# Optimization experiments

Hardware: AMD Instinct MI355X
Metric: run time of the kernel (lower is better)

Reference implementation:

```python
import jax, jax.numpy as jnp
import numpy as np

B, T, H, DK = 4, 2048, 16, 64
F = H * DK
CK, NL = 64, 16  # chunk_size, num left chunks
MIN_VAL = float(np.finfo(np.float16).min)


def chunk_mask(size, ck, nl):
    # row i attends cols [max((i//ck - nl)*ck, 0), (i//ck + 1)*ck)
    i = jnp.arange(size)
    start = jnp.maximum((i // ck - nl) * ck, 0)
    end = (i // ck + 1) * ck
    j = jnp.arange(size)
    return (j[None, :] >= start[:, None]) & (j[None, :] < end[:, None])


def setup_inputs() -> dict:
    rng = jax.random.key(0)
    ks = jax.random.split(rng, 14)
    s = 1.0 / np.sqrt(F)
    mask = jnp.broadcast_to(chunk_mask(T, CK, NL)[None], (B, T, T))  # padding mask all-True & chunk band
    return {
        "query": jax.random.normal(ks[0], (B, T, F), jnp.float32),
        "key": jax.random.normal(ks[1], (B, T, F), jnp.float32),
        "value": jax.random.normal(ks[2], (B, T, F), jnp.float32),
        "pos_emb": jax.random.normal(ks[3], (1, T, F), jnp.float32),
        "mask": mask,
        "Wq": jax.random.normal(ks[4], (F, F), jnp.float32) * s,
        "bq": jnp.zeros((F,), jnp.float32),
        "Wk": jax.random.normal(ks[5], (F, F), jnp.float32) * s,
        "bk": jnp.zeros((F,), jnp.float32),
        "Wv": jax.random.normal(ks[6], (F, F), jnp.float32) * s,
        "bv": jnp.zeros((F,), jnp.float32),
        "Wp": jax.random.normal(ks[7], (F, F), jnp.float32) * s,
        "Wo": jax.random.normal(ks[8], (F, F), jnp.float32) * s,
        "bo": jnp.zeros((F,), jnp.float32),
        "pos_bias_u": jax.random.normal(ks[9], (H, DK), jnp.float32) * 0.05,
        "pos_bias_v": jax.random.normal(ks[10], (H, DK), jnp.float32) * 0.05,
    }


def reference(query, key, value, pos_emb, mask, Wq, bq, Wk, bk, Wv, bv, Wp, Wo, bo, pos_bias_u, pos_bias_v):
    b, t1, _ = query.shape
    t2 = key.shape[1]
    q = (query @ Wq.T + bq).reshape(b, t1, H, DK)            # (b, t1, h, d)
    k = (key @ Wk.T + bk).reshape(b, t2, H, DK).transpose(0, 2, 1, 3)   # (b, h, t2, d)
    v = (value @ Wv.T + bv).reshape(b, t2, H, DK).transpose(0, 2, 1, 3)  # (b, h, t2, d)
    p = (pos_emb @ Wp.T).reshape(pos_emb.shape[0], -1, H, DK).transpose(0, 2, 1, 3)[0]  # (h, t2, d)
    # matrix_ac: content score with bias u; matrix_bd: position score with bias v (no rel_shift in forward)
    matrix_ac = jnp.einsum('bthd,bhsd->bhts', q + pos_bias_u, k)
    matrix_bd = jnp.einsum('bthd,hsd->bhts', q + pos_bias_v, p)
    scores = (matrix_ac + matrix_bd) / np.sqrt(DK)
    m = mask[:, None, :, :]                                   # (b, 1, t1, t2)
    scores = jnp.where(m, scores, MIN_VAL)
    attn = jax.nn.softmax(scores, axis=-1)
    attn = jnp.where(m, attn, 0.0)
    x = jnp.einsum('bhts,bhsd->bthd', attn, v).reshape(b, t1, F)
    return x @ Wo.T + bo
```

## Files before the change

### kernel.cpp

```cpp
#include <hip/hip_runtime.h>
#include <hip/hip_bf16.h>

#define B_ 4
#define T_ 2048
#define H_ 16
#define DK_ 64
#define F_ 1024
#define SCALE_LOG2 0.18033688011112042f

typedef __bf16 bf16x8 __attribute__((ext_vector_type(8)));
typedef __bf16 bf16x4 __attribute__((ext_vector_type(4)));
typedef float f32x4 __attribute__((ext_vector_type(4)));

__device__ __forceinline__ void async_cp16(const void* g, void* l) {
  __builtin_amdgcn_global_load_lds((const __attribute__((address_space(1))) void*)g,
                                   (__attribute__((address_space(3))) void*)l, 16, 0, 0);
}

struct CvtArgs {
  const float* src[9];
  __bf16* dst[9];
  int n[9];
};
__global__ void cvt_all(CvtArgs a) {
  int t = blockIdx.y;
  int i = (blockIdx.x * 256 + threadIdx.x) * 8;
  if (i >= a.n[t]) return;
  const float* in = a.src[t];
  __bf16* out = a.dst[t];
  float4 x = *(const float4*)(in + i);
  float4 y = *(const float4*)(in + i + 4);
  bf16x8 o;
  o[0] = (__bf16)x.x; o[1] = (__bf16)x.y; o[2] = (__bf16)x.z; o[3] = (__bf16)x.w;
  o[4] = (__bf16)y.x; o[5] = (__bf16)y.y; o[6] = (__bf16)y.z; o[7] = (__bf16)y.w;
  *(bf16x8*)(out + i) = o;
}

struct G8 {
  const __bf16* A[4];
  const __bf16* Bm[4];
  const float* bias[4];
  __bf16* out[4];
  int nx[4];
};

__global__ __launch_bounds__(512, 2) void gemm_qkvp8(G8 g) {
  const int z = blockIdx.z;
  if ((int)blockIdx.x >= g.nx[z]) return;
  constexpr int K = F_;
  constexpr int NT = K / 64;
  __shared__ __bf16 LDS[65536];
  const __bf16* __restrict__ A = g.A[z];
  const __bf16* __restrict__ Bmm = g.Bm[z];
  const float* __restrict__ bias = g.bias[z];
  __bf16* __restrict__ Co = g.out[z];
  const int tid = threadIdx.x;
  const int wave = tid >> 6, lane = tid & 63;
  const int mrow = lane & 15, quad = lane >> 4;
  const int wm = wave >> 2, wn = wave & 3;
  const long m0 = (long)blockIdx.y * 256;
  const long n0 = (long)blockIdx.x * 256;
  const int srow = tid >> 3;
  const int sslot = tid & 7;
  const int scol = ((sslot ^ (srow & 7)) * 8);
  const __bf16* sA = A + (m0 + srow) * K + scol;
  const __bf16* sB = Bmm + (n0 + srow) * K + scol;
  const int ldsw = wave * 512;
  const int csw0 = ((quad) ^ (mrow & 7)) * 8;
  const int csw1 = ((4 + quad) ^ (mrow & 7)) * 8;

#define STAGE_A(t_, h_)                                              \
  do {                                                               \
    __bf16* lb_ = &LDS[(((t_)&1) * 2 + (h_)) * 8192 + ldsw];         \
    const __bf16* ga_ = sA + (h_) * (128 * K) + (t_)*64;             \
    async_cp16(ga_, lb_);                                            \
    async_cp16(ga_ + 64 * K, lb_ + 4096);                            \
  } while (0)
#define STAGE_B(t_, h_)                                              \
  do {                                                               \
    __bf16* lb_ = &LDS[32768 + (((t_)&1) * 2 + (h_)) * 8192 + ldsw]; \
    const __bf16* gb_ = sB + (h_) * (128 * K) + (t_)*64;             \
    async_cp16(gb_, lb_);                                            \
    async_cp16(gb_ + 64 * K, lb_ + 4096);                            \
  } while (0)

  f32x4 acc[8][4] = {};
  bf16x8 af[8][2], bf[4][2];
  STAGE_A(0, 0); STAGE_A(0, 1); STAGE_B(0, 0); STAGE_B(0, 1);
  STAGE_A(1, 0); STAGE_A(1, 1);

#pragma unroll 2
  for (int t = 0; t < NT; ++t) {
    const int d = t & 1;
    const __bf16* Ab = &LDS[(d * 2 + wm) * 8192];
    const __bf16* Bb = &LDS[32768 + (d * 2 + (wn >> 1)) * 8192 + (wn & 1) * 4096];
    if (t + 1 < NT) {
      STAGE_B(t + 1, 0);
      asm volatile("s_waitcnt vmcnt(6)" ::: "memory");
    } else {
      asm volatile("s_waitcnt vmcnt(0)" ::: "memory");
    }
    __builtin_amdgcn_s_barrier();
#pragma unroll
    for (int fr = 0; fr < 4; ++fr) {
      af[fr][0] = *(const bf16x8*)&Ab[(fr * 16 + mrow) * 64 + csw0];
      af[fr][1] = *(const bf16x8*)&Ab[(fr * 16 + mrow) * 64 + csw1];
    }
#pragma unroll
    for (int fc = 0; fc < 2; ++fc) {
      bf[fc][0] = *(const bf16x8*)&Bb[(fc * 16 + mrow) * 64 + csw0];
      bf[fc][1] = *(const bf16x8*)&Bb[(fc * 16 + mrow) * 64 + csw1];
    }
    __builtin_amdgcn_s_setprio(1);
#pragma unroll
    for (int fr = 0; fr < 4; ++fr)
#pragma unroll
      for (int fc = 0; fc < 2; ++fc) {
        acc[fr][fc] = __builtin_amdgcn_mfma_f32_16x16x32_bf16(af[fr][0], bf[fc][0], acc[fr][fc], 0, 0, 0);
        acc[fr][fc] = __builtin_amdgcn_mfma_f32_16x16x32_bf16(af[fr][1], bf[fc][1], acc[fr][fc], 0, 0, 0);
      }
    __builtin_amdgcn_s_setprio(0);
    __builtin_amdgcn_s_barrier();
    if (t + 1 < NT) STAGE_B(t + 1, 1);
#pragma unroll
    for (int fr = 4; fr < 8; ++fr) {
      af[fr][0] = *(const bf16x8*)&Ab[(fr * 16 + mrow) * 64 + csw0];
      af[fr][1] = *(const bf16x8*)&Ab[(fr * 16 + mrow) * 64 + csw1];
    }
#pragma unroll
    for (int fc = 2; fc < 4; ++fc) {
      bf[fc][0] = *(const bf16x8*)&Bb[(fc * 16 + mrow) * 64 + csw0];
      bf[fc][1] = *(const bf16x8*)&Bb[(fc * 16 + mrow) * 64 + csw1];
    }
    __builtin_amdgcn_s_setprio(1);
#pragma unroll
    for (int fr = 4; fr < 8; ++fr)
#pragma unroll
      for (int fc = 2; fc < 4; ++fc) {
        acc[fr][fc] = __builtin_amdgcn_mfma_f32_16x16x32_bf16(af[fr][0], bf[fc][0], acc[fr][fc], 0, 0, 0);
        acc[fr][fc] = __builtin_amdgcn_mfma_f32_16x16x32_bf16(af[fr][1], bf[fc][1], acc[fr][fc], 0, 0, 0);
      }
    __builtin_amdgcn_s_setprio(0);
    __builtin_amdgcn_s_barrier();
    if (t + 2 < NT) STAGE_A(t + 2, 0);
    __builtin_amdgcn_s_setprio(1);
#pragma unroll
    for (int fr = 0; fr < 4; ++fr)
#pragma unroll
      for (int fc = 2; fc < 4; ++fc) {
        acc[fr][fc] = __builtin_amdgcn_mfma_f32_16x16x32_bf16(af[fr][0], bf[fc][0], acc[fr][fc], 0, 0, 0);
        acc[fr][fc] = __builtin_amdgcn_mfma_f32_16x16x32_bf16(af[fr][1], bf[fc][1], acc[fr][fc], 0, 0, 0);
      }
    __builtin_amdgcn_s_setprio(0);
    __builtin_amdgcn_s_barrier();
    if (t + 2 < NT) STAGE_A(t + 2, 1);
    __builtin_amdgcn_s_setprio(1);
#pragma unroll
    for (int fr = 4; fr < 8; ++fr)
#pragma unroll
      for (int fc = 0; fc < 2; ++fc) {
        acc[fr][fc] = __builtin_amdgcn_mfma_f32_16x16x32_bf16(af[fr][0], bf[fc][0], acc[fr][fc], 0, 0, 0);
        acc[fr][fc] = __builtin_amdgcn_mfma_f32_16x16x32_bf16(af[fr][1], bf[fc][1], acc[fr][fc], 0, 0, 0);
      }
    __builtin_amdgcn_s_setprio(0);
    __builtin_amdgcn_s_barrier();
  }
#undef STAGE_A
#undef STAGE_B

#pragma unroll
  for (int fr = 0; fr < 8; ++fr) {
    int frow = (int)m0 + wm * 128 + fr * 16 + quad * 4;
    float4 b4 = bias ? *(const float4*)&bias[frow] : make_float4(0.f, 0.f, 0.f, 0.f);
    int h = frow >> 6, dbase = frow & 63;
#pragma unroll
    for (int fc = 0; fc < 4; ++fc) {
      int token = (int)n0 + wn * 64 + fc * 16 + mrow;
      int bb = token >> 11, tt = token & 2047;
      bf16x4 pk;
      pk[0] = (__bf16)(acc[fr][fc][0] + b4.x);
      pk[1] = (__bf16)(acc[fr][fc][1] + b4.y);
      pk[2] = (__bf16)(acc[fr][fc][2] + b4.z);
      pk[3] = (__bf16)(acc[fr][fc][3] + b4.w);
      *(bf16x4*)&Co[(((long)(bb * H_ + h)) * T_ + tt) * DK_ + dbase] = pk;
    }
  }
}

__global__ __launch_bounds__(256) void gemm_out(
    const __bf16* __restrict__ A, const __bf16* __restrict__ Bm,
    float* __restrict__ Cout, const float* __restrict__ bias, int N, int K) {
  __shared__ __bf16 As[128 * 32];
  __shared__ __bf16 Bs[128 * 32];
  const int tid = threadIdx.x;
  const int wave = tid >> 6, lane = tid & 63;
  const int mrow = lane & 15, quad = lane >> 4;
  const long m0 = (long)blockIdx.y * 128, n0 = (long)blockIdx.x * 128;
  const int wr = (wave >> 1) * 64, wc = (wave & 1) * 64;
  const int srow = lane >> 2;
  const int scol = (lane & 3) * 8;
  f32x4 acc[4][4] = {};
  for (int k0 = 0; k0 < K; k0 += 32) {
    if (k0) __syncthreads();
    for (int ph = 0; ph < 2; ++ph) {
      int rb = ph * 64 + wave * 16;
      async_cp16(A + (m0 + rb + srow) * (long)K + k0 + scol, As + rb * 32);
      async_cp16(Bm + (n0 + rb + srow) * (long)K + k0 + scol, Bs + rb * 32);
    }
    __syncthreads();
    bf16x8 af[4], bf[4];
    for (int i = 0; i < 4; i++) af[i] = *(const bf16x8*)&As[(wr + i * 16 + mrow) * 32 + quad * 8];
    for (int j = 0; j < 4; j++) bf[j] = *(const bf16x8*)&Bs[(wc + j * 16 + mrow) * 32 + quad * 8];
    for (int i = 0; i < 4; i++)
      for (int j = 0; j < 4; j++)
        acc[i][j] = __builtin_amdgcn_mfma_f32_16x16x32_bf16(af[i], bf[j], acc[i][j], 0, 0, 0);
  }
  for (int i = 0; i < 4; i++) {
    int row = (int)m0 + wr + i * 16 + quad * 4;
    for (int j = 0; j < 4; j++) {
      int col = (int)n0 + wc + j * 16 + mrow;
      float bval = bias[col];
      for (int r = 0; r < 4; r++)
        Cout[(long)(row + r) * N + col] = acc[i][j][r] + bval;
    }
  }
}

__global__ __launch_bounds__(256) void prep(
    const __bf16* __restrict__ Ph, __bf16* __restrict__ Kh,
    const __bf16* __restrict__ Vh, __bf16* __restrict__ Vth,
    const float* __restrict__ u, const float* __restrict__ vb,
    float* __restrict__ biasC) {
  __shared__ __bf16 Vl[64 * 72];
  const int tc = blockIdx.x, h = blockIdx.y, b = blockIdx.z;
  const int tid = threadIdx.x;
  const int r4 = tid >> 2, c16 = (tid & 3) * 16;
  const long bh = b * H_ + h;
  const long kbase = (bh * T_ + tc * 64 + r4) * DK_ + c16;
  const long pbase = (((long)h) * T_ + tc * 64 + r4) * DK_ + c16;
  bf16x8 k0 = *(const bf16x8*)&Kh[kbase];
  bf16x8 k1 = *(const bf16x8*)&Kh[kbase + 8];
  bf16x8 p0 = *(const bf16x8*)&Ph[pbase];
  bf16x8 p1 = *(const bf16x8*)&Ph[pbase + 8];
  float4 u0 = *(const float4*)&u[h * 64 + c16];
  float4 u1 = *(const float4*)&u[h * 64 + c16 + 4];
  float4 u2 = *(const float4*)&u[h * 64 + c16 + 8];
  float4 u3 = *(const float4*)&u[h * 64 + c16 + 12];
  float4 v0 = *(const float4*)&vb[h * 64 + c16];
  float4 v1 = *(const float4*)&vb[h * 64 + c16 + 4];
  float4 v2 = *(const float4*)&vb[h * 64 + c16 + 8];
  float4 v3 = *(const float4*)&vb[h * 64 + c16 + 12];
  float s = 0.f;
  {
    const float uu[16] = {u0.x,u0.y,u0.z,u0.w,u1.x,u1.y,u1.z,u1.w,u2.x,u2.y,u2.z,u2.w,u3.x,u3.y,u3.z,u3.w};
    const float vv[16] = {v0.x,v0.y,v0.z,v0.w,v1.x,v1.y,v1.z,v1.w,v2.x,v2.y,v2.z,v2.w,v3.x,v3.y,v3.z,v3.w};
#pragma unroll
    for (int j = 0; j < 8; j++) {
      s += (float)k0[j] * uu[j] + (float)p0[j] * vv[j];
      s += (float)k1[j] * uu[8 + j] + (float)p1[j] * vv[8 + j];
    }
  }
  bf16x8 kp0, kp1;
#pragma unroll
  for (int j = 0; j < 8; j++) {
    kp0[j] = (__bf16)((float)k0[j] + (float)p0[j]);
    kp1[j] = (__bf16)((float)k1[j] + (float)p1[j]);
  }
  *(bf16x8*)&Kh[kbase] = kp0;
  *(bf16x8*)&Kh[kbase + 8] = kp1;
  s += __shfl_xor(s, 1);
  s += __shfl_xor(s, 2);
  if ((tid & 3) == 0) biasC[bh * T_ + tc * 64 + r4] = s * SCALE_LOG2;
  const long vbase = (bh * T_ + tc * 64 + r4) * DK_ + c16;
  bf16x8 vv0 = *(const bf16x8*)&Vh[vbase];
  bf16x8 vv1 = *(const bf16x8*)&Vh[vbase + 8];
  *(bf16x8*)&Vl[r4 * 72 + c16] = vv0;
  *(bf16x8*)&Vl[r4 * 72 + c16 + 8] = vv1;
  __syncthreads();
  const int d4 = tid >> 2, tcol = (tid & 3) * 16;
  bf16x8 o0, o1;
#pragma unroll
  for (int j = 0; j < 8; j++) {
    o0[j] = Vl[(tcol + j) * 72 + d4];
    o1[j] = Vl[(tcol + 8 + j) * 72 + d4];
  }
  long obase = (bh * DK_ + d4) * T_ + tc * 64 + tcol;
  *(bf16x8*)&Vth[obase] = o0;
  *(bf16x8*)&Vth[obase + 8] = o1;
}

template <int FULL>
__device__ __forceinline__ void attn_step2(
    int s0, long bh, int tid, int wave, int mrow, int quad,
    const __bf16* __restrict__ Kh, const __bf16* __restrict__ Vth,
    const float* __restrict__ Bp, const bf16x8 (&qf)[4][2],
    __bf16* Pl, __bf16* Vt, f32x4 accO[4], f32x4& accL) {
  __syncthreads();
  if (FULL) {
#pragma unroll
    for (int p = 0; p < 4; ++p) {
      int idx = tid + p * 256;
      int row = idx >> 4, colg = (idx & 15) * 8;
      *(bf16x8*)&Vt[row * 136 + colg] =
          *(const bf16x8*)&Vth[(bh * DK_ + row) * T_ + s0 + colg];
    }
  } else {
#pragma unroll
    for (int p = 0; p < 2; ++p) {
      int idx = tid + p * 256;
      int row = idx >> 3, colg = (idx & 7) * 8;
      *(bf16x8*)&Vt[row * 136 + colg] =
          *(const bf16x8*)&Vth[(bh * DK_ + row) * T_ + s0 + colg];
    }
  }
  if (FULL || wave < 2) {
    const int krow = s0 + wave * 32;
    bf16x8 kf[2][2];
#pragma unroll
    for (int nt = 0; nt < 2; ++nt)
#pragma unroll
      for (int kh = 0; kh < 2; ++kh)
        kf[nt][kh] = *(const bf16x8*)&Kh[(bh * T_ + krow + nt * 16 + mrow) * DK_ + kh * 32 + quad * 8];
    float bias01[2] = {Bp[krow + mrow], Bp[krow + 16 + mrow]};
    f32x4 s[4][2];
#pragma unroll
    for (int mt = 0; mt < 4; ++mt)
#pragma unroll
      for (int nt = 0; nt < 2; ++nt) {
        f32x4 a = {0.f, 0.f, 0.f, 0.f};
        a = __builtin_amdgcn_mfma_f32_16x16x32_bf16(qf[mt][0], kf[nt][0], a, 0, 0, 0);
        a = __builtin_amdgcn_mfma_f32_16x16x32_bf16(qf[mt][1], kf[nt][1], a, 0, 0, 0);
        s[mt][nt] = a;
      }
#pragma unroll
    for (int mt = 0; mt < 4; ++mt)
#pragma unroll
      for (int nt = 0; nt < 2; ++nt)
#pragma unroll
        for (int r = 0; r < 4; ++r) {
          float p = __builtin_amdgcn_exp2f(s[mt][nt][r] * SCALE_LOG2 + bias01[nt]);
          Pl[(mt * 16 + quad * 4 + r) * 136 + wave * 32 + nt * 16 + mrow] = (__bf16)p;
        }
  }
  __syncthreads();
  constexpr int NKT = FULL ? 4 : 2;
  bf16x8 ones;
#pragma unroll
  for (int j = 0; j < 8; ++j) ones[j] = (__bf16)1.0f;
  bf16x8 ap[NKT];
#pragma unroll
  for (int kt = 0; kt < NKT; ++kt)
    ap[kt] = *(const bf16x8*)&Pl[(wave * 16 + mrow) * 136 + kt * 32 + quad * 8];
#pragma unroll
  for (int kt = 0; kt < NKT; ++kt) {
    accL = __builtin_amdgcn_mfma_f32_16x16x32_bf16(ap[kt], ones, accL, 0, 0, 0);
#pragma unroll
    for (int nt = 0; nt < 4; ++nt) {
      bf16x8 bv = *(const bf16x8*)&Vt[(nt * 16 + mrow) * 136 + kt * 32 + quad * 8];
      accO[nt] = __builtin_amdgcn_mfma_f32_16x16x32_bf16(ap[kt], bv, accO[nt], 0, 0, 0);
    }
  }
}

__global__ __launch_bounds__(256) void attn_banded(
    const __bf16* __restrict__ Qh, const __bf16* __restrict__ Kh,
    const __bf16* __restrict__ Vth, const float* __restrict__ biasC,
    __bf16* __restrict__ X) {
  __shared__ __bf16 Pl[64 * 136];
  __shared__ __bf16 Vt[64 * 136];
  const int qc = blockIdx.x, h = blockIdx.y, b = blockIdx.z;
  const int tid = threadIdx.x, wave = tid >> 6, lane = tid & 63;
  const int mrow = lane & 15, quad = lane >> 4;
  const long bh = b * H_ + h;
  const int span = (qc >= 16 ? 17 : qc + 1);
  const int s_lo = (qc + 1 - span) * 64, s_hi = (qc + 1) * 64;
  const float* Bp = biasC + bh * T_;
  bf16x8 qf[4][2];
#pragma unroll
  for (int mt = 0; mt < 4; ++mt)
#pragma unroll
    for (int kh = 0; kh < 2; ++kh)
      qf[mt][kh] = *(const bf16x8*)&Qh[(bh * T_ + qc * 64 + mt * 16 + mrow) * DK_ + kh * 32 + quad * 8];
  f32x4 accO[4] = {};
  f32x4 accL = {0.f, 0.f, 0.f, 0.f};
  int s0 = s_lo;
  if (span & 1) {
    attn_step2<0>(s0, bh, tid, wave, mrow, quad, Kh, Vth, Bp, qf, Pl, Vt, accO, accL);
    s0 += 64;
  }
  for (; s0 < s_hi; s0 += 128)
    attn_step2<1>(s0, bh, tid, wave, mrow, quad, Kh, Vth, Bp, qf, Pl, Vt, accO, accL);
#pragma unroll
  for (int r = 0; r < 4; ++r) {
    float inv = 1.0f / accL[r];
    int t = qc * 64 + wave * 16 + quad * 4 + r;
#pragma unroll
    for (int nt = 0; nt < 4; ++nt)
      X[((long)(b * T_ + t) * H_ + h) * DK_ + nt * 16 + mrow] = (__bf16)(accO[nt][r] * inv);
  }
}

extern "C" void kernel_launch(void* const* d_in, const int* in_sizes, int n_in,
                              void* d_out, int out_size, void* d_ws, size_t ws_size,
                              hipStream_t stream) {
  (void)in_sizes; (void)n_in; (void)out_size; (void)ws_size;
  const float* query = (const float*)d_in[0];
  const float* key   = (const float*)d_in[1];
  const float* value = (const float*)d_in[2];
  const float* pos   = (const float*)d_in[3];
  const float* Wq = (const float*)d_in[5];
  const float* bq = (const float*)d_in[6];
  const float* Wk = (const float*)d_in[7];
  const float* bk = (const float*)d_in[8];
  const float* Wv = (const float*)d_in[9];
  const float* bv = (const float*)d_in[10];
  const float* Wp = (const float*)d_in[11];
  const float* Wo = (const float*)d_in[12];
  const float* bo = (const float*)d_in[13];
  const float* pu = (const float*)d_in[14];
  const float* pvb = (const float*)d_in[15];

  const long NQ = (long)B_ * T_ * F_;
  const long NP = (long)T_ * F_;
  const long NW = (long)F_ * F_;
  char* ws = (char*)d_ws;
  __bf16* qb  = (__bf16*)ws; ws += NQ * 2;
  __bf16* kb  = (__bf16*)ws; ws += NQ * 2;
  __bf16* vbm = (__bf16*)ws; ws += NQ * 2;
  __bf16* pb  = (__bf16*)ws; ws += NP * 2;
  __bf16* wqb = (__bf16*)ws; ws += NW * 2;
  __bf16* wkb = (__bf16*)ws; ws += NW * 2;
  __bf16* wvb = (__bf16*)ws; ws += NW * 2;
  __bf16* wpb = (__bf16*)ws; ws += NW * 2;
  __bf16* wob = (__bf16*)ws; ws += NW * 2;
  __bf16* Qh  = (__bf16*)ws; ws += NQ * 2;
  __bf16* Kh  = (__bf16*)ws; ws += NQ * 2;
  __bf16* Vh  = (__bf16*)ws; ws += NQ * 2;
  __bf16* Ph  = (__bf16*)ws; ws += NP * 2;
  float*  biasC = (float*)ws; ws += (long)B_ * H_ * T_ * 4;
  __bf16* Vth = kb;
  __bf16* Xb  = qb;

  {
    CvtArgs ca;
    ca.src[0] = query; ca.dst[0] = qb;  ca.n[0] = (int)NQ;
    ca.src[1] = key;   ca.dst[1] = kb;  ca.n[1] = (int)NQ;
    ca.src[2] = value; ca.dst[2] = vbm; ca.n[2] = (int)NQ;
    ca.src[3] = pos;   ca.dst[3] = pb;  ca.n[3] = (int)NP;
    ca.src[4] = Wq;    ca.dst[4] = wqb; ca.n[4] = (int)NW;
    ca.src[5] = Wk;    ca.dst[5] = wkb; ca.n[5] = (int)NW;
    ca.src[6] = Wv;    ca.dst[6] = wvb; ca.n[6] = (int)NW;
    ca.src[7] = Wp;    ca.dst[7] = wpb; ca.n[7] = (int)NW;
    ca.src[8] = Wo;    ca.dst[8] = wob; ca.n[8] = (int)NW;
    cvt_all<<<dim3(4096, 9), 256, 0, stream>>>(ca);
  }
  {
    G8 g;
    g.A[0] = wqb; g.Bm[0] = qb;  g.bias[0] = bq;      g.out[0] = Qh; g.nx[0] = 32;
    g.A[1] = wkb; g.Bm[1] = kb;  g.bias[1] = bk;      g.out[1] = Kh; g.nx[1] = 32;
    g.A[2] = wvb; g.Bm[2] = vbm; g.bias[2] = bv;      g.out[2] = Vh; g.nx[2] = 32;
    g.A[3] = wpb; g.Bm[3] = pb;  g.bias[3] = nullptr; g.out[3] = Ph; g.nx[3] = 8;
    gemm_qkvp8<<<dim3(32, 4, 4), 512, 0, stream>>>(g);
  }
  prep<<<dim3(32, 16, 4), 256, 0, stream>>>(Ph, Kh, Vh, Vth, pu, pvb, biasC);
  attn_banded<<<dim3(32, 16, 4), 256, 0, stream>>>(Qh, Kh, Vth, biasC, Xb);
  gemm_out<<<dim3(8, 64), 256, 0, stream>>>(Xb, wob, (float*)d_out, bo, F_, F_);
}
```

Before: 404.0 us.

## Software-pipeline banded attention with double-buffered P and direct V loads

```diff
diff --git a/kernel.cpp b/kernel.cpp
--- a/kernel.cpp
+++ b/kernel.cpp
@@ -289,91 +289,45 @@
   *(bf16x8*)&Vth[obase + 8] = o1;
 }
 
-template <int FULL>
-__device__ __forceinline__ void attn_step2(
-    int s0, long bh, int tid, int wave, int mrow, int quad,
-    const __bf16* __restrict__ Kh, const __bf16* __restrict__ Vth,
-    const float* __restrict__ Bp, const bf16x8 (&qf)[4][2],
-    __bf16* Pl, __bf16* Vt, f32x4 accO[4], f32x4& accL) {
-  __syncthreads();
-  if (FULL) {
-#pragma unroll
-    for (int p = 0; p < 4; ++p) {
-      int idx = tid + p * 256;
-      int row = idx >> 4, colg = (idx & 15) * 8;
-      *(bf16x8*)&Vt[row * 136 + colg] =
-          *(const bf16x8*)&Vth[(bh * DK_ + row) * T_ + s0 + colg];
-    }
-  } else {
-#pragma unroll
-    for (int p = 0; p < 2; ++p) {
-      int idx = tid + p * 256;
-      int row = idx >> 3, colg = (idx & 7) * 8;
-      *(bf16x8*)&Vt[row * 136 + colg] =
-          *(const bf16x8*)&Vth[(bh * DK_ + row) * T_ + s0 + colg];
-    }
-  }
-  if (FULL || wave < 2) {
-    const int krow = s0 + wave * 32;
-    bf16x8 kf[2][2];
-#pragma unroll
-    for (int nt = 0; nt < 2; ++nt)
-#pragma unroll
-      for (int kh = 0; kh < 2; ++kh)
-        kf[nt][kh] = *(const bf16x8*)&Kh[(bh * T_ + krow + nt * 16 + mrow) * DK_ + kh * 32 + quad * 8];
-    float bias01[2] = {Bp[krow + mrow], Bp[krow + 16 + mrow]};
-    f32x4 s[4][2];
-#pragma unroll
-    for (int mt = 0; mt < 4; ++mt)
-#pragma unroll
-      for (int nt = 0; nt < 2; ++nt) {
-        f32x4 a = {0.f, 0.f, 0.f, 0.f};
-        a = __builtin_amdgcn_mfma_f32_16x16x32_bf16(qf[mt][0], kf[nt][0], a, 0, 0, 0);
-        a = __builtin_amdgcn_mfma_f32_16x16x32_bf16(qf[mt][1], kf[nt][1], a, 0, 0, 0);
-        s[mt][nt] = a;
-      }
-#pragma unroll
-    for (int mt = 0; mt < 4; ++mt)
-#pragma unroll
-      for (int nt = 0; nt < 2; ++nt)
-#pragma unroll
-        for (int r = 0; r < 4; ++r) {
-          float p = __builtin_amdgcn_exp2f(s[mt][nt][r] * SCALE_LOG2 + bias01[nt]);
-          Pl[(mt * 16 + quad * 4 + r) * 136 + wave * 32 + nt * 16 + mrow] = (__bf16)p;
-        }
-  }
-  __syncthreads();
-  constexpr int NKT = FULL ? 4 : 2;
-  bf16x8 ones;
-#pragma unroll
-  for (int j = 0; j < 8; ++j) ones[j] = (__bf16)1.0f;
-  bf16x8 ap[NKT];
-#pragma unroll
-  for (int kt = 0; kt < NKT; ++kt)
-    ap[kt] = *(const bf16x8*)&Pl[(wave * 16 + mrow) * 136 + kt * 32 + quad * 8];
-#pragma unroll
-  for (int kt = 0; kt < NKT; ++kt) {
-    accL = __builtin_amdgcn_mfma_f32_16x16x32_bf16(ap[kt], ones, accL, 0, 0, 0);
-#pragma unroll
-    for (int nt = 0; nt < 4; ++nt) {
-      bf16x8 bv = *(const bf16x8*)&Vt[(nt * 16 + mrow) * 136 + kt * 32 + quad * 8];
-      accO[nt] = __builtin_amdgcn_mfma_f32_16x16x32_bf16(ap[kt], bv, accO[nt], 0, 0, 0);
-    }
-  }
-}
-
-__global__ __launch_bounds__(256) void attn_banded(
+__device__ __forceinline__ void qk_chunk(
+    int s0, long bh, int wave, int mrow, int quad,
+    const __bf16* __restrict__ Kh, const float* __restrict__ Bp,
+    const bf16x8 (&qf)[4][2], __bf16* __restrict__ Pb) {
+  const int krow = s0 + wave * 16;
+  const __bf16* kp = &Kh[(bh * T_ + krow + mrow) * DK_ + quad * 8];
+  bf16x8 kf0 = *(const bf16x8*)kp;
+  bf16x8 kf1 = *(const bf16x8*)(kp + 32);
+  float4 b4 = *(const float4*)&Bp[krow + quad * 4];
+  f32x4 s[4];
+#pragma unroll
+  for (int mt = 0; mt < 4; ++mt) {
+    f32x4 a = {0.f, 0.f, 0.f, 0.f};
+    a = __builtin_amdgcn_mfma_f32_16x16x32_bf16(kf0, qf[mt][0], a, 0, 0, 0);
+    a = __builtin_amdgcn_mfma_f32_16x16x32_bf16(kf1, qf[mt][1], a, 0, 0, 0);
+    s[mt] = a;
+  }
+#pragma unroll
+  for (int mt = 0; mt < 4; ++mt) {
+    bf16x4 pk;
+    pk[0] = (__bf16)__builtin_amdgcn_exp2f(s[mt][0] * SCALE_LOG2 + b4.x);
+    pk[1] = (__bf16)__builtin_amdgcn_exp2f(s[mt][1] * SCALE_LOG2 + b4.y);
+    pk[2] = (__bf16)__builtin_amdgcn_exp2f(s[mt][2] * SCALE_LOG2 + b4.z);
+    pk[3] = (__bf16)__builtin_amdgcn_exp2f(s[mt][3] * SCALE_LOG2 + b4.w);
+    *(bf16x4*)&Pb[(mt * 16 + mrow) * 72 + wave * 16 + quad * 4] = pk;
+  }
+}
+
+__global__ __launch_bounds__(256, 4) void attn_banded(
     const __bf16* __restrict__ Qh, const __bf16* __restrict__ Kh,
     const __bf16* __restrict__ Vth, const float* __restrict__ biasC,
     __bf16* __restrict__ X) {
-  __shared__ __bf16 Pl[64 * 136];
-  __shared__ __bf16 Vt[64 * 136];
+  __shared__ __bf16 Pl[2][64 * 72];
   const int qc = blockIdx.x, h = blockIdx.y, b = blockIdx.z;
   const int tid = threadIdx.x, wave = tid >> 6, lane = tid & 63;
   const int mrow = lane & 15, quad = lane >> 4;
   const long bh = b * H_ + h;
   const int span = (qc >= 16 ? 17 : qc + 1);
-  const int s_lo = (qc + 1 - span) * 64, s_hi = (qc + 1) * 64;
+  const int s_lo = (qc + 1 - span) * 64;
   const float* Bp = biasC + bh * T_;
   bf16x8 qf[4][2];
 #pragma unroll
@@ -383,13 +337,36 @@
       qf[mt][kh] = *(const bf16x8*)&Qh[(bh * T_ + qc * 64 + mt * 16 + mrow) * DK_ + kh * 32 + quad * 8];
   f32x4 accO[4] = {};
   f32x4 accL = {0.f, 0.f, 0.f, 0.f};
-  int s0 = s_lo;
-  if (span & 1) {
-    attn_step2<0>(s0, bh, tid, wave, mrow, quad, Kh, Vth, Bp, qf, Pl, Vt, accO, accL);
-    s0 += 64;
-  }
-  for (; s0 < s_hi; s0 += 128)
-    attn_step2<1>(s0, bh, tid, wave, mrow, quad, Kh, Vth, Bp, qf, Pl, Vt, accO, accL);
+  bf16x8 ones;
+#pragma unroll
+  for (int j = 0; j < 8; ++j) ones[j] = (__bf16)1.0f;
+
+  qk_chunk(s_lo, bh, wave, mrow, quad, Kh, Bp, qf, &Pl[0][0]);
+
+  const __bf16* Vb = &Vth[(bh * DK_ + mrow) * T_];
+  for (int c = 0; c < span; ++c) {
+    const int s0 = s_lo + c * 64;
+    __syncthreads();
+    bf16x8 bv[2][4];
+#pragma unroll
+    for (int kt = 0; kt < 2; ++kt)
+#pragma unroll
+      for (int nt = 0; nt < 4; ++nt)
+        bv[kt][nt] = *(const bf16x8*)&Vb[(long)(nt * 16) * T_ + s0 + kt * 32 + quad * 8];
+    bf16x8 ap[2];
+#pragma unroll
+    for (int kt = 0; kt < 2; ++kt)
+      ap[kt] = *(const bf16x8*)&Pl[c & 1][(wave * 16 + mrow) * 72 + kt * 32 + quad * 8];
+    if (c + 1 < span)
+      qk_chunk(s0 + 64, bh, wave, mrow, quad, Kh, Bp, qf, &Pl[(c + 1) & 1][0]);
+#pragma unroll
+    for (int kt = 0; kt < 2; ++kt) {
+      accL = __builtin_amdgcn_mfma_f32_16x16x32_bf16(ap[kt], ones, accL, 0, 0, 0);
+#pragma unroll
+      for (int nt = 0; nt < 4; ++nt)
+        accO[nt] = __builtin_amdgcn_mfma_f32_16x16x32_bf16(ap[kt], bv[kt][nt], accO[nt], 0, 0, 0);
+    }
+  }
 #pragma unroll
   for (int r = 0; r < 4; ++r) {
     float inv = 1.0f / accL[r];
```

Measured after the change: 477.9 us. 18.3% more time.

## Register-prefetch next K/V/bias tile in banded attention loop with masked partial step

Applied to the files above, without the earlier changes.

```diff
diff --git a/kernel.cpp b/kernel.cpp
--- a/kernel.cpp
+++ b/kernel.cpp
@@ -289,80 +289,7 @@
   *(bf16x8*)&Vth[obase + 8] = o1;
 }
 
-template <int FULL>
-__device__ __forceinline__ void attn_step2(
-    int s0, long bh, int tid, int wave, int mrow, int quad,
-    const __bf16* __restrict__ Kh, const __bf16* __restrict__ Vth,
-    const float* __restrict__ Bp, const bf16x8 (&qf)[4][2],
-    __bf16* Pl, __bf16* Vt, f32x4 accO[4], f32x4& accL) {
-  __syncthreads();
-  if (FULL) {
-#pragma unroll
-    for (int p = 0; p < 4; ++p) {
-      int idx = tid + p * 256;
-      int row = idx >> 4, colg = (idx & 15) * 8;
-      *(bf16x8*)&Vt[row * 136 + colg] =
-          *(const bf16x8*)&Vth[(bh * DK_ + row) * T_ + s0 + colg];
-    }
-  } else {
-#pragma unroll
-    for (int p = 0; p < 2; ++p) {
-      int idx = tid + p * 256;
-      int row = idx >> 3, colg = (idx & 7) * 8;
-      *(bf16x8*)&Vt[row * 136 + colg] =
-          *(const bf16x8*)&Vth[(bh * DK_ + row) * T_ + s0 + colg];
-    }
-  }
-  if (FULL || wave < 2) {
-    const int krow = s0 + wave * 32;
-    bf16x8 kf[2][2];
-#pragma unroll
-    for (int nt = 0; nt < 2; ++nt)
-#pragma unroll
-      for (int kh = 0; kh < 2; ++kh)
-        kf[nt][kh] = *(const bf16x8*)&Kh[(bh * T_ + krow + nt * 16 + mrow) * DK_ + kh * 32 + quad * 8];
-    float bias01[2] = {Bp[krow + mrow], Bp[krow + 16 + mrow]};
-    f32x4 s[4][2];
-#pragma unroll
-    for (int mt = 0; mt < 4; ++mt)
-#pragma unroll
-      for (int nt = 0; nt < 2; ++nt) {
-        f32x4 a = {0.f, 0.f, 0.f, 0.f};
-        a = __builtin_amdgcn_mfma_f32_16x16x32_bf16(qf[mt][0], kf[nt][0], a, 0, 0, 0);
-        a = __builtin_amdgcn_mfma_f32_16x16x32_bf16(qf[mt][1], kf[nt][1], a, 0, 0, 0);
-        s[mt][nt] = a;
-      }
-#pragma unroll
-    for (int mt = 0; mt < 4; ++mt)
-#pragma unroll
-      for (int nt = 0; nt < 2; ++nt)
-#pragma unroll
-        for (int r = 0; r < 4; ++r) {
-          float p = __builtin_amdgcn_exp2f(s[mt][nt][r] * SCALE_LOG2 + bias01[nt]);
-          Pl[(mt * 16 + quad * 4 + r) * 136 + wave * 32 + nt * 16 + mrow] = (__bf16)p;
-        }
-  }
-  __syncthreads();
-  constexpr int NKT = FULL ? 4 : 2;
-  bf16x8 ones;
-#pragma unroll
-  for (int j = 0; j < 8; ++j) ones[j] = (__bf16)1.0f;
-  bf16x8 ap[NKT];
-#pragma unroll
-  for (int kt = 0; kt < NKT; ++kt)
-    ap[kt] = *(const bf16x8*)&Pl[(wave * 16 + mrow) * 136 + kt * 32 + quad * 8];
-#pragma unroll
-  for (int kt = 0; kt < NKT; ++kt) {
-    accL = __builtin_amdgcn_mfma_f32_16x16x32_bf16(ap[kt], ones, accL, 0, 0, 0);
-#pragma unroll
-    for (int nt = 0; nt < 4; ++nt) {
-      bf16x8 bv = *(const bf16x8*)&Vt[(nt * 16 + mrow) * 136 + kt * 32 + quad * 8];
-      accO[nt] = __builtin_amdgcn_mfma_f32_16x16x32_bf16(ap[kt], bv, accO[nt], 0, 0, 0);
-    }
-  }
-}
-
-__global__ __launch_bounds__(256) void attn_banded(
+__global__ __launch_bounds__(256, 3) void attn_banded(
     const __bf16* __restrict__ Qh, const __bf16* __restrict__ Kh,
     const __bf16* __restrict__ Vth, const float* __restrict__ biasC,
     __bf16* __restrict__ X) {
@@ -374,6 +301,7 @@
   const long bh = b * H_ + h;
   const int span = (qc >= 16 ? 17 : qc + 1);
   const int s_lo = (qc + 1 - span) * 64, s_hi = (qc + 1) * 64;
+  const int steps = (span + 1) >> 1;
   const float* Bp = biasC + bh * T_;
   bf16x8 qf[4][2];
 #pragma unroll
@@ -383,13 +311,110 @@
       qf[mt][kh] = *(const bf16x8*)&Qh[(bh * T_ + qc * 64 + mt * 16 + mrow) * DK_ + kh * 32 + quad * 8];
   f32x4 accO[4] = {};
   f32x4 accL = {0.f, 0.f, 0.f, 0.f};
-  int s0 = s_lo;
-  if (span & 1) {
-    attn_step2<0>(s0, bh, tid, wave, mrow, quad, Kh, Vth, Bp, qf, Pl, Vt, accO, accL);
-    s0 += 64;
-  }
-  for (; s0 < s_hi; s0 += 128)
-    attn_step2<1>(s0, bh, tid, wave, mrow, quad, Kh, Vth, Bp, qf, Pl, Vt, accO, accL);
+  const __bf16* Kbase = Kh + bh * T_ * DK_;
+  const __bf16* Vbase = Vth + bh * DK_ * T_;
+
+#define LOAD_K(S, DST)                                                                \
+  do {                                                                                \
+    _Pragma("unroll") for (int nt_ = 0; nt_ < 2; ++nt_) {                             \
+      int k_ = (S) + wave * 32 + nt_ * 16 + mrow;                                     \
+      int kc_ = k_ < 0 ? 0 : k_;                                                      \
+      _Pragma("unroll") for (int kh_ = 0; kh_ < 2; ++kh_)                             \
+          DST[nt_][kh_] = *(const bf16x8*)&Kbase[(long)kc_ * DK_ + kh_ * 32 + quad * 8]; \
+    }                                                                                 \
+  } while (0)
+#define LOAD_V(S, DST)                                                                \
+  do {                                                                                \
+    _Pragma("unroll") for (int p_ = 0; p_ < 4; ++p_) {                                \
+      int idx_ = tid + p_ * 256;                                                      \
+      int row_ = idx_ >> 4, colg_ = (idx_ & 15) * 8;                                  \
+      int k_ = (S) + colg_;                                                           \
+      int kc_ = k_ < 0 ? 0 : k_;                                                      \
+      DST[p_] = *(const bf16x8*)&Vbase[(long)row_ * T_ + kc_];                        \
+    }                                                                                 \
+  } while (0)
+#define LOAD_B(S, DST)                                                                \
+  do {                                                                                \
+    _Pragma("unroll") for (int nt_ = 0; nt_ < 2; ++nt_) {                             \
+      int k_ = (S) + wave * 32 + nt_ * 16 + mrow;                                     \
+      int kc_ = k_ < 0 ? 0 : k_;                                                      \
+      DST[nt_] = Bp[kc_];                                                             \
+    }                                                                                 \
+  } while (0)
+
+  bf16x8 kfc[2][2], kfn[2][2], vrc[4], vrn[4];
+  float bc[2], bn[2];
+  int s0 = s_hi - steps * 128;
+  LOAD_K(s0, kfc);
+  LOAD_V(s0, vrc);
+  LOAD_B(s0, bc);
+
+  for (int st = 0; st < steps; ++st, s0 += 128) {
+    __syncthreads();
+#pragma unroll
+    for (int p = 0; p < 4; ++p) {
+      int idx = tid + p * 256;
+      int row = idx >> 4, colg = (idx & 15) * 8;
+      *(bf16x8*)&Vt[row * 136 + colg] = vrc[p];
+    }
+    f32x4 s[4][2];
+#pragma unroll
+    for (int mt = 0; mt < 4; ++mt)
+#pragma unroll
+      for (int nt = 0; nt < 2; ++nt) {
+        f32x4 a = {0.f, 0.f, 0.f, 0.f};
+        a = __builtin_amdgcn_mfma_f32_16x16x32_bf16(qf[mt][0], kfc[nt][0], a, 0, 0, 0);
+        a = __builtin_amdgcn_mfma_f32_16x16x32_bf16(qf[mt][1], kfc[nt][1], a, 0, 0, 0);
+        s[mt][nt] = a;
+      }
+    if (st + 1 < steps) {
+      LOAD_K(s0 + 128, kfn);
+      LOAD_V(s0 + 128, vrn);
+      LOAD_B(s0 + 128, bn);
+    }
+#pragma unroll
+    for (int nt = 0; nt < 2; ++nt) {
+      int key = s0 + wave * 32 + nt * 16 + mrow;
+      float bb = (key >= s_lo) ? bc[nt] : -1000.0f;
+#pragma unroll
+      for (int mt = 0; mt < 4; ++mt)
+#pragma unroll
+        for (int r = 0; r < 4; ++r) {
+          float p = __builtin_amdgcn_exp2f(s[mt][nt][r] * SCALE_LOG2 + bb);
+          Pl[(mt * 16 + quad * 4 + r) * 136 + wave * 32 + nt * 16 + mrow] = (__bf16)p;
+        }
+    }
+    __syncthreads();
+    bf16x8 ones;
+#pragma unroll
+    for (int j = 0; j < 8; ++j) ones[j] = (__bf16)1.0f;
+    bf16x8 ap[4];
+#pragma unroll
+    for (int kt = 0; kt < 4; ++kt)
+      ap[kt] = *(const bf16x8*)&Pl[(wave * 16 + mrow) * 136 + kt * 32 + quad * 8];
+#pragma unroll
+    for (int kt = 0; kt < 4; ++kt) {
+      accL = __builtin_amdgcn_mfma_f32_16x16x32_bf16(ap[kt], ones, accL, 0, 0, 0);
+#pragma unroll
+      for (int nt = 0; nt < 4; ++nt) {
+        bf16x8 bv = *(const bf16x8*)&Vt[(nt * 16 + mrow) * 136 + kt * 32 + quad * 8];
+        accO[nt] = __builtin_amdgcn_mfma_f32_16x16x32_bf16(ap[kt], bv, accO[nt], 0, 0, 0);
+      }
+    }
+    if (st + 1 < steps) {
+#pragma unroll
+      for (int nt = 0; nt < 2; ++nt) {
+        bc[nt] = bn[nt];
+#pragma unroll
+        for (int kh = 0; kh < 2; ++kh) kfc[nt][kh] = kfn[nt][kh];
+      }
+#pragma unroll
+      for (int p = 0; p < 4; ++p) vrc[p] = vrn[p];
+    }
+  }
+#undef LOAD_K
+#undef LOAD_V
+#undef LOAD_B
 #pragma unroll
   for (int r = 0; r < 4; ++r) {
     float inv = 1.0f / accL[r];
```

Result: slower. 418.9 us (+3.7%).

## Process two query chunks per attention block to share K/V tile loads

Applied to the files above, without the earlier changes.

```diff
diff --git a/kernel.cpp b/kernel.cpp
--- a/kernel.cpp
+++ b/kernel.cpp
@@ -289,111 +289,103 @@
   *(bf16x8*)&Vth[obase + 8] = o1;
 }
 
-template <int FULL>
-__device__ __forceinline__ void attn_step2(
-    int s0, long bh, int tid, int wave, int mrow, int quad,
-    const __bf16* __restrict__ Kh, const __bf16* __restrict__ Vth,
-    const float* __restrict__ Bp, const bf16x8 (&qf)[4][2],
-    __bf16* Pl, __bf16* Vt, f32x4 accO[4], f32x4& accL) {
-  __syncthreads();
-  if (FULL) {
-#pragma unroll
-    for (int p = 0; p < 4; ++p) {
-      int idx = tid + p * 256;
+__global__ __launch_bounds__(512) void attn_banded(
+    const __bf16* __restrict__ Qh, const __bf16* __restrict__ Kh,
+    const __bf16* __restrict__ Vth, const float* __restrict__ biasC,
+    __bf16* __restrict__ X) {
+  __shared__ __bf16 Pl[128 * 136];
+  __shared__ __bf16 Vt[64 * 136];
+  const int d = (int)blockIdx.x + 16 * ((int)blockIdx.y + 16 * (int)blockIdx.z);
+  const int w = (d & 7) * 128 + (d >> 3);
+  const int qc2 = w & 15, h = (w >> 4) & 15, b = w >> 8;
+  const int tid = threadIdx.x, wave = tid >> 6, lane = tid & 63;
+  const int mrow = lane & 15, quad = lane >> 4;
+  const long bh = b * H_ + h;
+  const int qhalf = wave >> 2;
+  const int c2 = 2 * qc2 + qhalf;
+  const int startH = (c2 >= 16 ? (c2 - 16) * 64 : 0);
+  const int endH = (c2 + 1) * 64;
+  const int s_lo = (2 * qc2 >= 16 ? (2 * qc2 - 16) * 64 : 0);
+  const int s_hi = (2 * qc2 + 2) * 64;
+  const float* Bp = biasC + bh * T_;
+  bf16x8 qf[4][2];
+#pragma unroll
+  for (int mt = 0; mt < 4; ++mt)
+#pragma unroll
+    for (int kh = 0; kh < 2; ++kh)
+      qf[mt][kh] = *(const bf16x8*)&Qh[(bh * T_ + qc2 * 128 + qhalf * 64 + mt * 16 + mrow) * DK_ + kh * 32 + quad * 8];
+  f32x4 accO[4] = {};
+  f32x4 accL = {0.f, 0.f, 0.f, 0.f};
+  bf16x8 ones;
+#pragma unroll
+  for (int j = 0; j < 8; ++j) ones[j] = (__bf16)1.0f;
+
+  for (int s0 = s_lo; s0 < s_hi; s0 += 128) {
+    __syncthreads();
+#pragma unroll
+    for (int p = 0; p < 2; ++p) {
+      int idx = tid + p * 512;
       int row = idx >> 4, colg = (idx & 15) * 8;
       *(bf16x8*)&Vt[row * 136 + colg] =
           *(const bf16x8*)&Vth[(bh * DK_ + row) * T_ + s0 + colg];
     }
-  } else {
-#pragma unroll
-    for (int p = 0; p < 2; ++p) {
-      int idx = tid + p * 256;
-      int row = idx >> 3, colg = (idx & 7) * 8;
-      *(bf16x8*)&Vt[row * 136 + colg] =
-          *(const bf16x8*)&Vth[(bh * DK_ + row) * T_ + s0 + colg];
-    }
-  }
-  if (FULL || wave < 2) {
-    const int krow = s0 + wave * 32;
-    bf16x8 kf[2][2];
-#pragma unroll
-    for (int nt = 0; nt < 2; ++nt)
-#pragma unroll
-      for (int kh = 0; kh < 2; ++kh)
-        kf[nt][kh] = *(const bf16x8*)&Kh[(bh * T_ + krow + nt * 16 + mrow) * DK_ + kh * 32 + quad * 8];
-    float bias01[2] = {Bp[krow + mrow], Bp[krow + 16 + mrow]};
-    f32x4 s[4][2];
-#pragma unroll
-    for (int mt = 0; mt < 4; ++mt)
-#pragma unroll
-      for (int nt = 0; nt < 2; ++nt) {
-        f32x4 a = {0.f, 0.f, 0.f, 0.f};
-        a = __builtin_amdgcn_mfma_f32_16x16x32_bf16(qf[mt][0], kf[nt][0], a, 0, 0, 0);
-        a = __builtin_amdgcn_mfma_f32_16x16x32_bf16(qf[mt][1], kf[nt][1], a, 0, 0, 0);
-        s[mt][nt] = a;
+    const int kchunk = s0 + ((wave & 3) >> 1) * 64;
+    const int krow = s0 + (wave & 3) * 32;
+    if (kchunk >= startH && kchunk < endH) {
+      bf16x8 kf[2][2];
+#pragma unroll
+      for (int nt = 0; nt < 2; ++nt)
+#pragma unroll
+        for (int kh = 0; kh < 2; ++kh)
+          kf[nt][kh] = *(const bf16x8*)&Kh[(bh * T_ + krow + nt * 16 + mrow) * DK_ + kh * 32 + quad * 8];
+      float bias01[2] = {Bp[krow + mrow], Bp[krow + 16 + mrow]};
+      f32x4 s[4][2];
+#pragma unroll
+      for (int mt = 0; mt < 4; ++mt)
+#pragma unroll
+        for (int nt = 0; nt < 2; ++nt) {
+          f32x4 a = {0.f, 0.f, 0.f, 0.f};
+          a = __builtin_amdgcn_mfma_f32_16x16x32_bf16(qf[mt][0], kf[nt][0], a, 0, 0, 0);
+          a = __builtin_amdgcn_mfma_f32_16x16x32_bf16(qf[mt][1], kf[nt][1], a, 0, 0, 0);
+          s[mt][nt] = a;
+        }
+#pragma unroll
+      for (int mt = 0; mt < 4; ++mt)
+#pragma unroll
+        for (int nt = 0; nt < 2; ++nt)
+#pragma unroll
+          for (int r = 0; r < 4; ++r) {
+            float p = __builtin_amdgcn_exp2f(s[mt][nt][r] * SCALE_LOG2 + bias01[nt]);
+            Pl[(qhalf * 64 + mt * 16 + quad * 4 + r) * 136 + (wave & 3) * 32 + nt * 16 + mrow] = (__bf16)p;
+          }
+    } else {
+#pragma unroll
+      for (int mt = 0; mt < 4; ++mt)
+#pragma unroll
+        for (int nt = 0; nt < 2; ++nt)
+#pragma unroll
+          for (int r = 0; r < 4; ++r)
+            Pl[(qhalf * 64 + mt * 16 + quad * 4 + r) * 136 + (wave & 3) * 32 + nt * 16 + mrow] = (__bf16)0.0f;
+    }
+    __syncthreads();
+    bf16x8 ap[4];
+#pragma unroll
+    for (int kt = 0; kt < 4; ++kt)
+      ap[kt] = *(const bf16x8*)&Pl[(wave * 16 + mrow) * 136 + kt * 32 + quad * 8];
+#pragma unroll
+    for (int kt = 0; kt < 4; ++kt) {
+      accL = __builtin_amdgcn_mfma_f32_16x16x32_bf16(ap[kt], ones, accL, 0, 0, 0);
+#pragma unroll
+      for (int nt = 0; nt < 4; ++nt) {
+        bf16x8 bv = *(const bf16x8*)&Vt[(nt * 16 + mrow) * 136 + kt * 32 + quad * 8];
+        accO[nt] = __builtin_amdgcn_mfma_f32_16x16x32_bf16(ap[kt], bv, accO[nt], 0, 0, 0);
       }
-#pragma unroll
-    for (int mt = 0; mt < 4; ++mt)
-#pragma unroll
-      for (int nt = 0; nt < 2; ++nt)
-#pragma unroll
-        for (int r = 0; r < 4; ++r) {
-          float p = __builtin_amdgcn_exp2f(s[mt][nt][r] * SCALE_LOG2 + bias01[nt]);
-          Pl[(mt * 16 + quad * 4 + r) * 136 + wave * 32 + nt * 16 + mrow] = (__bf16)p;
-        }
-  }
-  __syncthreads();
-  constexpr int NKT = FULL ? 4 : 2;
-  bf16x8 ones;
-#pragma unroll
-  for (int j = 0; j < 8; ++j) ones[j] = (__bf16)1.0f;
-  bf16x8 ap[NKT];
-#pragma unroll
-  for (int kt = 0; kt < NKT; ++kt)
-    ap[kt] = *(const bf16x8*)&Pl[(wave * 16 + mrow) * 136 + kt * 32 + quad * 8];
-#pragma unroll
-  for (int kt = 0; kt < NKT; ++kt) {
-    accL = __builtin_amdgcn_mfma_f32_16x16x32_bf16(ap[kt], ones, accL, 0, 0, 0);
-#pragma unroll
-    for (int nt = 0; nt < 4; ++nt) {
-      bf16x8 bv = *(const bf16x8*)&Vt[(nt * 16 + mrow) * 136 + kt * 32 + quad * 8];
-      accO[nt] = __builtin_amdgcn_mfma_f32_16x16x32_bf16(ap[kt], bv, accO[nt], 0, 0, 0);
-    }
-  }
-}
-
-__global__ __launch_bounds__(256) void attn_banded(
-    const __bf16* __restrict__ Qh, const __bf16* __restrict__ Kh,
-    const __bf16* __restrict__ Vth, const float* __restrict__ biasC,
-    __bf16* __restrict__ X) {
-  __shared__ __bf16 Pl[64 * 136];
-  __shared__ __bf16 Vt[64 * 136];
-  const int qc = blockIdx.x, h = blockIdx.y, b = blockIdx.z;
-  const int tid = threadIdx.x, wave = tid >> 6, lane = tid & 63;
-  const int mrow = lane & 15, quad = lane >> 4;
-  const long bh = b * H_ + h;
-  const int span = (qc >= 16 ? 17 : qc + 1);
-  const int s_lo = (qc + 1 - span) * 64, s_hi = (qc + 1) * 64;
-  const float* Bp = biasC + bh * T_;
-  bf16x8 qf[4][2];
-#pragma unroll
-  for (int mt = 0; mt < 4; ++mt)
-#pragma unroll
-    for (int kh = 0; kh < 2; ++kh)
-      qf[mt][kh] = *(const bf16x8*)&Qh[(bh * T_ + qc * 64 + mt * 16 + mrow) * DK_ + kh * 32 + quad * 8];
-  f32x4 accO[4] = {};
-  f32x4 accL = {0.f, 0.f, 0.f, 0.f};
-  int s0 = s_lo;
-  if (span & 1) {
-    attn_step2<0>(s0, bh, tid, wave, mrow, quad, Kh, Vth, Bp, qf, Pl, Vt, accO, accL);
-    s0 += 64;
-  }
-  for (; s0 < s_hi; s0 += 128)
-    attn_step2<1>(s0, bh, tid, wave, mrow, quad, Kh, Vth, Bp, qf, Pl, Vt, accO, accL);
+    }
+  }
 #pragma unroll
   for (int r = 0; r < 4; ++r) {
     float inv = 1.0f / accL[r];
-    int t = qc * 64 + wave * 16 + quad * 4 + r;
+    int t = qc2 * 128 + wave * 16 + quad * 4 + r;
 #pragma unroll
     for (int nt = 0; nt < 4; ++nt)
       X[((long)(b * T_ + t) * H_ + h) * DK_ + nt * 16 + mrow] = (__bf16)(accO[nt][r] * inv);
@@ -463,6 +455,6 @@
     gemm_qkvp8<<<dim3(32, 4, 4), 512, 0, stream>>>(g);
   }
   prep<<<dim3(32, 16, 4), 256, 0, stream>>>(Ph, Kh, Vh, Vth, pu, pvb, biasC);
-  attn_banded<<<dim3(32, 16, 4), 256, 0, stream>>>(Qh, Kh, Vth, biasC, Xb);
+  attn_banded<<<dim3(16, 16, 4), 512, 0, stream>>>(Qh, Kh, Vth, biasC, Xb);
   gemm_out<<<dim3(8, 64), 256, 0, stream>>>(Xb, wob, (float*)d_out, bo, F_, F_);
 }
```

Result: faster. 384.5 us (-4.8%).
